# Kernel tuning notes

Hardware: AMD Instinct MI355X
Metric: run time of the kernel (lower is better)

Reference implementation:

```python
import jax, jax.numpy as jnp
import numpy as np

B = 16384      # games
BS = 19        # board size
N2 = BS * BS   # 361
G = 8          # groups per board
S = 4          # stones per group
R = B * G      # total groups
K = R * S      # total stones
M = N2         # hash history length (H*W*history_factor)
I32MIN = np.iinfo(np.int32).min
I32MAX = np.iinfo(np.int32).max
NEG = jnp.float32(-1e9)


def setup_inputs() -> dict:
    key = jax.random.key(0)
    ks = jax.random.split(key, 10)
    logits = jax.random.normal(ks[0], (B, BS, BS), dtype=jnp.float32)
    legal_mask = jax.random.uniform(ks[1], (B, BS, BS)) < 0.7
    current_player = jax.random.randint(ks[2], (B,), 0, 2, dtype=jnp.int32)
    current_hash = jax.random.randint(ks[3], (B,), 0, I32MAX, dtype=jnp.int32)
    hash_history = jax.random.randint(ks[4], (B, M), 0, I32MAX, dtype=jnp.int32)
    move_count = jax.random.randint(ks[5], (B,), 0, M, dtype=jnp.int32)
    ZposT = jax.random.randint(ks[6], (3, N2), 0, I32MAX, dtype=jnp.int32)
    stone_global_index = jax.random.randint(ks[7], (K,), 0, N2, dtype=jnp.int32)
    stone_global_pointer = jnp.arange(R + 1, dtype=jnp.int32) * S          # CSR: stones per group
    group_global_pointer_per_board = jnp.arange(B + 1, dtype=jnp.int32) * G  # CSR: groups per board
    cap_idx = jax.random.randint(ks[8], (B, N2, 4), 0, G, dtype=jnp.int32)
    cap_on = jax.random.uniform(ks[9], (B, N2, 4)) < 0.05
    captured_group_local_index = jnp.where(cap_on, cap_idx, jnp.int32(-1))
    return {
        "logits": logits,
        "legal_mask": legal_mask,
        "current_player": current_player,
        "current_hash": current_hash,
        "hash_history": hash_history,
        "move_count": move_count,
        "ZposT": ZposT,
        "stone_global_index": stone_global_index,
        "stone_global_pointer": stone_global_pointer,
        "group_global_pointer_per_board": group_global_pointer_per_board,
        "captured_group_local_index": captured_group_local_index,
    }


def reference(logits, legal_mask, current_player, current_hash, hash_history,
              move_count, ZposT, stone_global_index, stone_global_pointer,
              group_global_pointer_per_board, captured_group_local_index):
    Bn, H, W = legal_mask.shape
    Rn = stone_global_pointer.shape[0] - 1
    Kn = stone_global_index.shape[0]
    z_empty, z_black, z_white = ZposT[0], ZposT[1], ZposT[2]

    # Placement delta: empty -> current player's stone, for every candidate point. (B, N2)
    placement_delta = z_empty[None, :] ^ jnp.where(
        (current_player == 0)[:, None], z_black[None, :], z_white[None, :])

    # Map each group -> board, each stone -> group (CSR expansion).
    groups_per_board = group_global_pointer_per_board[1:] - group_global_pointer_per_board[:-1]
    group_board = jnp.repeat(jnp.arange(Bn, dtype=jnp.int32), groups_per_board,
                             total_repeat_length=Rn)
    stones_per_group = stone_global_pointer[1:] - stone_global_pointer[:-1]
    group_for_stone = jnp.repeat(jnp.arange(Rn, dtype=jnp.int32), stones_per_group,
                                 total_repeat_length=Kn)
    stone_board = group_board[group_for_stone]

    # Per-stone removal delta: opponent stone -> empty.
    opp_for_stone = (1 - current_player)[stone_board]           # (K,)
    si = stone_global_index.astype(jnp.int32)
    z_opp = ZposT[1 + opp_for_stone, si]
    per_stone_delta = z_opp ^ z_empty[si]                        # (K,) int32

    # Segmented XOR reduction over each group's stones via XOR prefix scan.
    prefix = jax.lax.associative_scan(jnp.bitwise_xor, per_stone_delta)
    start = stone_global_pointer[:-1]
    end = stone_global_pointer[1:]
    end_val = prefix[jnp.clip(end - 1, 0)]
    start_val = jnp.where(start > 0, prefix[jnp.clip(start - 1, 0)], jnp.int32(0))
    group_xor = end_val ^ start_val                              # (R,) per-group removal delta

    # Gather capture deltas for up to 4 captured neighbor groups per candidate move.
    offs = group_global_pointer_per_board[:-1][:, None, None]    # (B,1,1)
    flat_ids = jnp.clip(captured_group_local_index, 0) + offs    # (B,N2,4)
    cap_vals = jnp.where(captured_group_local_index >= 0, group_xor[flat_ids], jnp.int32(0))
    capture_delta = cap_vals[..., 0] ^ cap_vals[..., 1] ^ cap_vals[..., 2] ^ cap_vals[..., 3]

    candidate = current_hash[:, None] ^ placement_delta ^ capture_delta  # (B, N2)

    # Super-ko repeat detection against hash history (mask, sort, searchsorted).
    Mh = hash_history.shape[1]
    valid = jnp.arange(Mh, dtype=jnp.int32)[None, :] < jnp.minimum(move_count, Mh)[:, None]
    masked_hist = jnp.where(valid, hash_history, jnp.int32(I32MIN))
    sorted_hist = jnp.sort(masked_hist, axis=1)
    idx = jnp.clip(
        jax.vmap(lambda h, c: jnp.searchsorted(h, c, side='right'))(sorted_hist, candidate) - 1,
        0)
    found = jnp.take_along_axis(sorted_hist, idx, axis=1)
    repeat = (found == candidate).reshape(Bn, H, W)

    final_mask = legal_mask & ~repeat
    return jnp.where(final_mask, logits, NEG)
```

## Files before the change

### kernel.cpp

```cpp
#include <hip/hip_runtime.h>
#include <stdint.h>

#define N2 361
#define TBL 2048
#define TBL_MASK 2047u
#define EMPTY_SLOT 0x80000000u

__global__ __launch_bounds__(256) void go_repeat_mask_kernel(
    const float* __restrict__ logits,
    const void*  __restrict__ legal_raw,
    const int*   __restrict__ current_player,
    const int*   __restrict__ current_hash,
    const int*   __restrict__ hash_history,
    const int*   __restrict__ move_count,
    const int*   __restrict__ ZposT,
    const int*   __restrict__ stone_global_index,
    const int*   __restrict__ stone_global_pointer,
    const int*   __restrict__ group_global_pointer,
    const int4*  __restrict__ captured4,
    float*       __restrict__ out,
    int packed_bits)
{
    __shared__ unsigned s_table[TBL];
    __shared__ int s_gx[8];
    __shared__ int s_flags;

    const int b   = blockIdx.x;
    const int tid = threadIdx.x;

    if (tid == 0) s_flags = 0;
    for (int i = tid; i < TBL; i += 256) s_table[i] = EMPTY_SLOT;
    __syncthreads();

    unsigned f = 0;
    if (!packed_bits) {
        const unsigned* lw = (const unsigned*)legal_raw;
        const unsigned w0 = ((unsigned)b * N2) >> 2;
        const unsigned w1 = ((unsigned)b * N2 + N2 + 3u) >> 2;
        for (unsigned w = w0 + tid; w < w1; w += 256) {
            const unsigned v = lw[w];
            #pragma unroll
            for (int j = 0; j < 4; ++j) {
                const unsigned bv = (v >> (8 * j)) & 0xFFu;
                if (bv > 1u) f |= 1u;
                if (j != 0 && bv != 0u) f |= 2u;
            }
            const unsigned h0 = v & 0xFFFFu, h1 = v >> 16;
            if ((h0 != 0u && h0 != 0x3F80u) || (h1 != 0u && h1 != 0x3F80u)) f |= 4u;
            if (h0 == 0x3F80u) f |= 8u;
        }
        if (f) atomicOr(&s_flags, (int)f);
    }

    const int      cp = current_player[b];
    const unsigned ch = (unsigned)current_hash[b];
    int cnt = move_count[b];
    cnt = cnt < 0 ? 0 : (cnt > N2 ? N2 : cnt);

    if (tid < 8) {
        const int g0 = group_global_pointer[b];
        const int g1 = group_global_pointer[b + 1];
        const int r  = g0 + tid;
        unsigned gx = 0u;
        if (r < g1) {
            const int s0 = stone_global_pointer[r];
            const int s1 = stone_global_pointer[r + 1];
            const int opprow = (2 - cp) * N2;
            for (int k = s0; k < s1; ++k) {
                const int si = stone_global_index[k];
                gx ^= (unsigned)ZposT[opprow + si] ^ (unsigned)ZposT[si];
            }
        }
        s_gx[tid] = (int)gx;
    }

    const int* hist = hash_history + (size_t)b * N2;
    for (int i = tid; i < cnt; i += 256) {
        const unsigned v = (unsigned)hist[i];
        unsigned slot = v & TBL_MASK;
        while (true) {
            const unsigned old = atomicCAS(&s_table[slot], EMPTY_SLOT, v);
            if (old == EMPTY_SLOT || old == v) break;
            slot = (slot + 1) & TBL_MASK;
        }
    }
    __syncthreads();

    int fmt;
    if (packed_bits) fmt = 4;
    else {
        const int flags = s_flags;
        if (!(flags & 1)) fmt = (flags & 2) ? 1 : 0;
        else if (!(flags & 4)) fmt = (flags & 8) ? 2 : 3;
        else fmt = 1;
    }

    const size_t bbase = (size_t)b * N2;
    const int prow = (1 + cp) * N2;
    for (int n = tid; n < N2; n += 256) {
        const size_t q = bbase + n;
        const int4 cap = captured4[q];

        unsigned capd = 0u;
        if (cap.x >= 0) capd ^= (unsigned)s_gx[cap.x & 7];
        if (cap.y >= 0) capd ^= (unsigned)s_gx[cap.y & 7];
        if (cap.z >= 0) capd ^= (unsigned)s_gx[cap.z & 7];
        if (cap.w >= 0) capd ^= (unsigned)s_gx[cap.w & 7];

        const unsigned pd   = (unsigned)ZposT[n] ^ (unsigned)ZposT[prow + n];
        const unsigned cand = ch ^ pd ^ capd;

        bool repeat = false;
        unsigned slot = cand & TBL_MASK;
        while (true) {
            const unsigned v = s_table[slot];
            if (v == cand) { repeat = true; break; }
            if (v == EMPTY_SLOT) break;
            slot = (slot + 1) & TBL_MASK;
        }

        bool legal;
        if      (fmt == 0) legal = ((const int*)legal_raw)[q] != 0;
        else if (fmt == 1) legal = ((const uint8_t*)legal_raw)[q] != 0;
        else if (fmt == 2) legal = ((const uint16_t*)legal_raw)[q] != 0;
        else if (fmt == 3) legal = ((const unsigned*)legal_raw)[q] != 0;
        else legal = ((((const uint8_t*)legal_raw)[q >> 3] >> (q & 7)) & 1) != 0;

        out[q] = (legal && !repeat) ? logits[q] : -998244352.0f;
    }
}

extern "C" void kernel_launch(void* const* d_in, const int* in_sizes, int n_in,
                              void* d_out, int out_size, void* d_ws, size_t ws_size,
                              hipStream_t stream) {
    const float* logits  = (const float*)d_in[0];
    const void*  legal   = (const void*)d_in[1];
    const int*   cur_pl  = (const int*)d_in[2];
    const int*   cur_h   = (const int*)d_in[3];
    const int*   hist    = (const int*)d_in[4];
    const int*   mcount  = (const int*)d_in[5];
    const int*   zpos    = (const int*)d_in[6];
    const int*   sgi     = (const int*)d_in[7];
    const int*   sgp     = (const int*)d_in[8];
    const int*   ggp     = (const int*)d_in[9];
    const int4*  cap4    = (const int4*)d_in[10];
    float*       out     = (float*)d_out;

    const int B = in_sizes[2];
    const int packed = (in_sizes[1] != in_sizes[0]);

    go_repeat_mask_kernel<<<B, 256, 0, stream>>>(
        logits, legal, cur_pl, cur_h, hist, mcount, zpos,
        sgi, sgp, ggp, cap4, out, packed);
}
```

Baseline: 263.4 us.

## Use 128-thread blocks with all global loads hoisted before hash table build

Each block now uses 128 threads, and each thread handles three board cells. All per-cell global loads (history, capture indices, logits, legal mask) are issued up front so their latency overlaps the table setup. Legal-mask format detection now uses wave ballots over the first words of the buffer instead of a per-board shared-memory atomic scan. The shared hash table is halved to 1024 slots and outputs use nontemporal stores. This trades longer probe chains and a coarser format check for fewer serial memory round-trips per block.

New measurement: 223.6 us. 15.1% less time.

```diff
diff --git a/kernel.cpp b/kernel.cpp
--- a/kernel.cpp
+++ b/kernel.cpp
@@ -2,11 +2,12 @@
 #include <stdint.h>
 
 #define N2 361
-#define TBL 2048
-#define TBL_MASK 2047u
+#define TBL 1024
+#define TBL_MASK 1023u
 #define EMPTY_SLOT 0x80000000u
-
-__global__ __launch_bounds__(256) void go_repeat_mask_kernel(
+#define NEGV -998244352.0f
+
+__global__ __launch_bounds__(128) void go_repeat_mask_kernel(
     const float* __restrict__ logits,
     const void*  __restrict__ legal_raw,
     const int*   __restrict__ current_player,
@@ -23,110 +24,161 @@
 {
     __shared__ unsigned s_table[TBL];
     __shared__ int s_gx[8];
-    __shared__ int s_flags;
 
     const int b   = blockIdx.x;
     const int tid = threadIdx.x;
-
-    if (tid == 0) s_flags = 0;
-    for (int i = tid; i < TBL; i += 256) s_table[i] = EMPTY_SLOT;
+    const size_t bbase = (size_t)b * N2;
+
+    const int      cp  = current_player[b];
+    const unsigned ch  = (unsigned)current_hash[b];
+    int            cnt = move_count[b];
+
+    const int iC = (tid + 256 < N2) ? (tid + 256) : (N2 - 1);
+
+    const int* hist = hash_history + bbase;
+    const int h0 = hist[tid];
+    const int h1 = hist[tid + 128];
+    const int h2 = hist[iC];
+
+    const int4 capA = captured4[bbase + tid];
+    const int4 capB = captured4[bbase + tid + 128];
+    const int4 capC = captured4[bbase + iC];
+
+    const float lgA = logits[bbase + tid];
+    const float lgB = logits[bbase + tid + 128];
+    const float lgC = logits[bbase + iC];
+
+    const unsigned* lwd = (const unsigned*)legal_raw;
+    const int lane = tid & 63;
+    const unsigned dv0 = lwd[lane];
+    const unsigned dv1 = (lane < 27) ? lwd[64 + lane] : 0u;
+
+    int g0 = 0, g1 = 0, sp0 = 0, sp1 = 0;
+    if (tid < 32) {
+        g0 = group_global_pointer[b];
+        g1 = group_global_pointer[b + 1];
+        const int r = g0 + (tid >> 2);
+        if (r < g1) {
+            sp0 = stone_global_pointer[r];
+            sp1 = stone_global_pointer[r + 1];
+        }
+    }
+
+    auto classify = [](unsigned v) -> unsigned {
+        unsigned f = 0;
+        #pragma unroll
+        for (int j = 0; j < 4; ++j) {
+            const unsigned bv = (v >> (8 * j)) & 0xFFu;
+            if (bv > 1u) f |= 1u;
+            if (j != 0 && bv != 0u) f |= 2u;
+        }
+        const unsigned ha = v & 0xFFFFu, hb = v >> 16;
+        if ((ha && ha != 0x3F80u) || (hb && hb != 0x3F80u)) f |= 4u;
+        if (ha == 0x3F80u) f |= 8u;
+        return f;
+    };
+    unsigned fcl = classify(dv0);
+    if (lane < 27) fcl |= classify(dv1);
+    unsigned fa = 0;
+    fa |= __ballot(fcl & 1u) ? 1u : 0u;
+    fa |= __ballot(fcl & 2u) ? 2u : 0u;
+    fa |= __ballot(fcl & 4u) ? 4u : 0u;
+    fa |= __ballot(fcl & 8u) ? 8u : 0u;
+
+    int fmt;
+    if (packed_bits) fmt = 4;
+    else if (!(fa & 1u)) fmt = 0;
+    else if (!(fa & 4u)) fmt = (fa & 8u) ? 2 : 0;
+    else fmt = 1;
+
+    unsigned legA, legB, legC;
+    {
+        const size_t qA = bbase + tid, qB = bbase + tid + 128, qC = bbase + iC;
+        if (fmt == 0) {
+            const unsigned* p = (const unsigned*)legal_raw;
+            legA = p[qA]; legB = p[qB]; legC = p[qC];
+        } else if (fmt == 1) {
+            const uint8_t* p = (const uint8_t*)legal_raw;
+            legA = p[qA]; legB = p[qB]; legC = p[qC];
+        } else if (fmt == 2) {
+            const uint16_t* p = (const uint16_t*)legal_raw;
+            legA = p[qA]; legB = p[qB]; legC = p[qC];
+        } else {
+            const uint8_t* p = (const uint8_t*)legal_raw;
+            legA = (p[qA >> 3] >> (qA & 7)) & 1u;
+            legB = (p[qB >> 3] >> (qB & 7)) & 1u;
+            legC = (p[qC >> 3] >> (qC & 7)) & 1u;
+        }
+    }
+
+    if (tid < 32) {
+        unsigned gx = 0u;
+        const int j = tid & 3;
+        const int opprow = (2 - cp) * N2;
+        for (int k = sp0 + j; k < sp1; k += 4) {
+            const int si = stone_global_index[k];
+            gx ^= (unsigned)ZposT[opprow + si] ^ (unsigned)ZposT[si];
+        }
+        gx ^= __shfl_xor(gx, 1);
+        gx ^= __shfl_xor(gx, 2);
+        if (j == 0) s_gx[tid >> 2] = (int)gx;
+    }
+
+    #pragma unroll
+    for (int i = 0; i < TBL / 128; ++i) s_table[tid + i * 128] = EMPTY_SLOT;
+
+    cnt = cnt < 0 ? 0 : (cnt > N2 ? N2 : cnt);
     __syncthreads();
 
-    unsigned f = 0;
-    if (!packed_bits) {
-        const unsigned* lw = (const unsigned*)legal_raw;
-        const unsigned w0 = ((unsigned)b * N2) >> 2;
-        const unsigned w1 = ((unsigned)b * N2 + N2 + 3u) >> 2;
-        for (unsigned w = w0 + tid; w < w1; w += 256) {
-            const unsigned v = lw[w];
-            #pragma unroll
-            for (int j = 0; j < 4; ++j) {
-                const unsigned bv = (v >> (8 * j)) & 0xFFu;
-                if (bv > 1u) f |= 1u;
-                if (j != 0 && bv != 0u) f |= 2u;
-            }
-            const unsigned h0 = v & 0xFFFFu, h1 = v >> 16;
-            if ((h0 != 0u && h0 != 0x3F80u) || (h1 != 0u && h1 != 0x3F80u)) f |= 4u;
-            if (h0 == 0x3F80u) f |= 8u;
-        }
-        if (f) atomicOr(&s_flags, (int)f);
-    }
-
-    const int      cp = current_player[b];
-    const unsigned ch = (unsigned)current_hash[b];
-    int cnt = move_count[b];
-    cnt = cnt < 0 ? 0 : (cnt > N2 ? N2 : cnt);
-
-    if (tid < 8) {
-        const int g0 = group_global_pointer[b];
-        const int g1 = group_global_pointer[b + 1];
-        const int r  = g0 + tid;
-        unsigned gx = 0u;
-        if (r < g1) {
-            const int s0 = stone_global_pointer[r];
-            const int s1 = stone_global_pointer[r + 1];
-            const int opprow = (2 - cp) * N2;
-            for (int k = s0; k < s1; ++k) {
-                const int si = stone_global_index[k];
-                gx ^= (unsigned)ZposT[opprow + si] ^ (unsigned)ZposT[si];
-            }
-        }
-        s_gx[tid] = (int)gx;
-    }
-
-    const int* hist = hash_history + (size_t)b * N2;
-    for (int i = tid; i < cnt; i += 256) {
-        const unsigned v = (unsigned)hist[i];
+    auto insert = [&](unsigned v) {
         unsigned slot = v & TBL_MASK;
         while (true) {
             const unsigned old = atomicCAS(&s_table[slot], EMPTY_SLOT, v);
             if (old == EMPTY_SLOT || old == v) break;
             slot = (slot + 1) & TBL_MASK;
         }
-    }
+    };
+    if (tid < cnt)       insert((unsigned)h0);
+    if (tid + 128 < cnt) insert((unsigned)h1);
+    if (tid + 256 < cnt) insert((unsigned)h2);
     __syncthreads();
 
-    int fmt;
-    if (packed_bits) fmt = 4;
-    else {
-        const int flags = s_flags;
-        if (!(flags & 1)) fmt = (flags & 2) ? 1 : 0;
-        else if (!(flags & 4)) fmt = (flags & 8) ? 2 : 3;
-        else fmt = 1;
-    }
-
-    const size_t bbase = (size_t)b * N2;
     const int prow = (1 + cp) * N2;
-    for (int n = tid; n < N2; n += 256) {
-        const size_t q = bbase + n;
-        const int4 cap = captured4[q];
-
-        unsigned capd = 0u;
-        if (cap.x >= 0) capd ^= (unsigned)s_gx[cap.x & 7];
-        if (cap.y >= 0) capd ^= (unsigned)s_gx[cap.y & 7];
-        if (cap.z >= 0) capd ^= (unsigned)s_gx[cap.z & 7];
-        if (cap.w >= 0) capd ^= (unsigned)s_gx[cap.w & 7];
-
-        const unsigned pd   = (unsigned)ZposT[n] ^ (unsigned)ZposT[prow + n];
-        const unsigned cand = ch ^ pd ^ capd;
-
-        bool repeat = false;
+    auto probe = [&](unsigned cand) -> bool {
         unsigned slot = cand & TBL_MASK;
         while (true) {
             const unsigned v = s_table[slot];
-            if (v == cand) { repeat = true; break; }
-            if (v == EMPTY_SLOT) break;
+            if (v == cand) return true;
+            if (v == EMPTY_SLOT) return false;
             slot = (slot + 1) & TBL_MASK;
         }
-
-        bool legal;
-        if      (fmt == 0) legal = ((const int*)legal_raw)[q] != 0;
-        else if (fmt == 1) legal = ((const uint8_t*)legal_raw)[q] != 0;
-        else if (fmt == 2) legal = ((const uint16_t*)legal_raw)[q] != 0;
-        else if (fmt == 3) legal = ((const unsigned*)legal_raw)[q] != 0;
-        else legal = ((((const uint8_t*)legal_raw)[q >> 3] >> (q & 7)) & 1) != 0;
-
-        out[q] = (legal && !repeat) ? logits[q] : -998244352.0f;
+    };
+    auto capxor = [&](int4 c) -> unsigned {
+        unsigned d = 0u;
+        if (c.x >= 0) d ^= (unsigned)s_gx[c.x & 7];
+        if (c.y >= 0) d ^= (unsigned)s_gx[c.y & 7];
+        if (c.z >= 0) d ^= (unsigned)s_gx[c.z & 7];
+        if (c.w >= 0) d ^= (unsigned)s_gx[c.w & 7];
+        return d;
+    };
+
+    {
+        const int n = tid;
+        const unsigned cand = ch ^ (unsigned)ZposT[n] ^ (unsigned)ZposT[prow + n] ^ capxor(capA);
+        const float v = (legA && !probe(cand)) ? lgA : NEGV;
+        __builtin_nontemporal_store(v, &out[bbase + n]);
+    }
+    {
+        const int n = tid + 128;
+        const unsigned cand = ch ^ (unsigned)ZposT[n] ^ (unsigned)ZposT[prow + n] ^ capxor(capB);
+        const float v = (legB && !probe(cand)) ? lgB : NEGV;
+        __builtin_nontemporal_store(v, &out[bbase + n]);
+    }
+    if (tid < N2 - 256) {
+        const int n = tid + 256;
+        const unsigned cand = ch ^ (unsigned)ZposT[n] ^ (unsigned)ZposT[prow + n] ^ capxor(capC);
+        const float v = (legC && !probe(cand)) ? lgC : NEGV;
+        __builtin_nontemporal_store(v, &out[bbase + n]);
     }
 }
 
@@ -149,7 +201,7 @@
     const int B = in_sizes[2];
     const int packed = (in_sizes[1] != in_sizes[0]);
 
-    go_repeat_mask_kernel<<<B, 256, 0, stream>>>(
+    go_repeat_mask_kernel<<<B, 128, 0, stream>>>(
         logits, legal, cur_pl, cur_h, hist, mcount, zpos,
         sgi, sgp, ggp, cap4, out, packed);
 }
```
